# Kernel tuning notes

Measured on AMD Instinct MI355X. Metric: run time of the kernel, lower is better.

The kernel has to match this reference:

```python
import jax, jax.numpy as jnp
import numpy as np
import math

B, W, D_IN, H = 64, 512, 300, 512

def setup_inputs() -> dict:
    key = jax.random.key(0)
    ks = jax.random.split(key, 8)
    s = 1.0 / math.sqrt(D_IN)
    return {
        "char_vectors": jax.random.normal(ks[0], (B, W, D_IN), jnp.float32),
        "word_vectors": jax.random.normal(ks[1], (B, W, D_IN), jnp.float32),
        "Wk": jax.random.uniform(ks[2], (D_IN, H), jnp.float32, -s, s),
        "bk": jnp.zeros((H,), jnp.float32),
        "Wq": jax.random.uniform(ks[3], (D_IN, H), jnp.float32, -s, s),
        "bq": jnp.zeros((H,), jnp.float32),
        "Wv": jax.random.uniform(ks[4], (D_IN, H), jnp.float32, -s, s),
        "bv": jnp.zeros((H,), jnp.float32),
    }

def reference(char_vectors, word_vectors, Wk, bk, Wq, bq, Wv, bv):
    # Stack word/char reps per word -> [B, W, 2, H]
    def proj(Wm, bm):
        return jnp.stack([word_vectors @ Wm + bm, char_vectors @ Wm + bm], axis=2)
    K = proj(Wk, bk)
    Q = proj(Wq, bq)
    V = proj(Wv, bv)
    temp = jnp.sqrt(jnp.asarray(H, jnp.float32))
    # tiny 2x2 attention per word, fully batched (dropout off = eval mode)
    attn = jnp.einsum("bwqh,bwkh->bwqk", Q, K) / temp
    attn = jax.nn.softmax(attn, axis=-1)
    out = jnp.einsum("bwqk,bwkh->bwqh", attn, V)  # [B, W, 2, H]
    return out.reshape(B, W, 2 * H)
```

## Files before the change

kernel.cpp:

```cpp
#include <hip/hip_runtime.h>

#define D 300
#define HDIM 512
#define ROWS 128
#define WPB 64
#define NKS 20
#define NCH 48
#define CH_BYTES 20480
#define CH_ELEMS 10240
#define SEGW 5

typedef __attribute__((ext_vector_type(16))) float f32x16;
typedef __attribute__((ext_vector_type(4))) float f32x4;
typedef __attribute__((ext_vector_type(8))) short bf16x8;

__device__ inline unsigned short f2bf(float f) {
  unsigned int u = __float_as_uint(f);
  unsigned int r = (u + 0x7fffu + ((u >> 16) & 1u)) >> 16;
  return (unsigned short)r;
}

__device__ inline void gload_lds16(const void* g, void* l) {
  __builtin_amdgcn_global_load_lds(
      (const __attribute__((address_space(1))) unsigned int*)g,
      (__attribute__((address_space(3))) unsigned int*)l, 16, 0, 0);
}

__global__ __launch_bounds__(512) void prep_weights(
    const float* __restrict__ Wq, const float* __restrict__ Wk,
    const float* __restrict__ Wv, unsigned short* __restrict__ wt) {
  int idx = blockIdx.x * 512 + threadIdx.x;
  if (idx >= NCH * CH_ELEMS) return;
  int c = idx / CH_ELEMS, r2 = idx - c * CH_ELEMS;
  int ks = r2 >> 9, r3 = r2 & 511;
  int kh = r3 >> 8, r4 = r3 & 255;
  int col = r4 >> 3, e = r4 & 7;
  int k = ks * 16 + kh * 8 + e;
  const float* M; int gcol;
  if (c < 32) { M = (c & 1) ? Wk : Wq; gcol = (c >> 1) * 32 + col; }
  else        { M = Wv; gcol = (c - 32) * 32 + col; }
  float v = (k < D) ? M[k * HDIM + gcol] : 0.0f;
  wt[idx] = f2bf(v);
}

__global__ __launch_bounds__(256) void fused_attn(
    const float* __restrict__ charv, const float* __restrict__ wordv,
    const unsigned short* __restrict__ wt,
    const float* __restrict__ bk, const float* __restrict__ bq,
    const float* __restrict__ bv, float* __restrict__ out) {
  extern __shared__ char lds[];
  float* biasL = (float*)(lds + 3 * CH_BYTES);
  float* sS    = biasL + 1536;
  float* sAt   = sS;

  const int tid  = threadIdx.x;
  const int wid  = tid >> 6;
  const int lane = tid & 63;
  const int lo5  = lane & 31;
  const int hi   = lane >> 5;

  auto stage = [&](int t) {
    const char* src = (const char*)wt + (long)t * CH_BYTES + wid * (SEGW * 1024) + lane * 16;
    char* dst = lds + (t % 3) * CH_BYTES + wid * (SEGW * 1024);
#pragma unroll
    for (int j = 0; j < SEGW; ++j)
      gload_lds16(src + j * 1024, dst + j * 1024);
  };

  for (int i = tid; i < 1536; i += 256) {
    float v = (i < 512) ? bq[i] : ((i < 1024) ? bk[i - 512] : bv[i - 1024]);
    biasL[i] = v;
  }
  bf16x8 a[NKS];
  {
    int row = blockIdx.x * ROWS + wid * 32 + lo5;
    const float* rp = ((row & 1) ? charv : wordv) + (row >> 1) * D;
#pragma unroll
    for (int ks = 0; ks < NKS; ++ks) {
      int k0 = ks * 16 + hi * 8;
      float4 lo = {0.f, 0.f, 0.f, 0.f}, hif = {0.f, 0.f, 0.f, 0.f};
      if (k0 + 8 <= D) {
        lo  = *(const float4*)(rp + k0);
        hif = *(const float4*)(rp + k0 + 4);
      } else if (k0 < D) {
        lo  = *(const float4*)(rp + k0);
      }
      bf16x8 v;
      v[0] = (short)f2bf(lo.x);  v[1] = (short)f2bf(lo.y);
      v[2] = (short)f2bf(lo.z);  v[3] = (short)f2bf(lo.w);
      v[4] = (short)f2bf(hif.x); v[5] = (short)f2bf(hif.y);
      v[6] = (short)f2bf(hif.z); v[7] = (short)f2bf(hif.w);
      a[ks] = v;
    }
  }
  stage(0);
  stage(1);

  float p[32];
#pragma unroll
  for (int t = 0; t < 32; ++t) p[t] = 0.f;

  f32x16 accQ;

  for (int g = 0; g < 16; ++g) {
    asm volatile("s_waitcnt vmcnt(5)" ::: "memory");
    asm volatile("s_waitcnt lgkmcnt(0)" ::: "memory");
    __builtin_amdgcn_s_barrier();
    stage(2 * g + 2);
    {
      const char* base = lds + ((2 * g) % 3) * CH_BYTES + hi * 512 + lo5 * 16;
      float bqv = biasL[g * 32 + lo5];
#pragma unroll
      for (int r = 0; r < 16; ++r) accQ[r] = bqv;
#pragma unroll
      for (int ks = 0; ks < NKS; ++ks) {
        bf16x8 qb = *(const bf16x8*)(base + ks * 1024);
        accQ = __builtin_amdgcn_mfma_f32_32x32x16_bf16(a[ks], qb, accQ, 0, 0, 0);
      }
    }
    asm volatile("s_waitcnt vmcnt(5)" ::: "memory");
    asm volatile("s_waitcnt lgkmcnt(0)" ::: "memory");
    __builtin_amdgcn_s_barrier();
    stage(2 * g + 3);
    {
      const char* base = lds + ((2 * g + 1) % 3) * CH_BYTES + hi * 512 + lo5 * 16;
      float bkv = biasL[512 + g * 32 + lo5];
      f32x16 accK;
#pragma unroll
      for (int r = 0; r < 16; ++r) accK[r] = bkv;
#pragma unroll
      for (int ks = 0; ks < NKS; ++ks) {
        bf16x8 kb = *(const bf16x8*)(base + ks * 1024);
        accK = __builtin_amdgcn_mfma_f32_32x32x16_bf16(a[ks], kb, accK, 0, 0, 0);
      }
#pragma unroll
      for (int tt = 0; tt < 8; ++tt)
#pragma unroll
        for (int i = 0; i < 2; ++i)
#pragma unroll
          for (int j = 0; j < 2; ++j)
            p[tt * 4 + i * 2 + j] += accQ[2 * tt + i] * accK[2 * tt + j];
    }
  }

#pragma unroll
  for (int t = 0; t < 32; ++t) {
    float v = p[t];
    v += __shfl_xor(v, 1);
    v += __shfl_xor(v, 2);
    v += __shfl_xor(v, 4);
    v += __shfl_xor(v, 8);
    v += __shfl_xor(v, 16);
    p[t] = v;
  }
  if (lo5 == 0) {
#pragma unroll
    for (int tt = 0; tt < 8; ++tt) {
      int w = wid * 16 + (tt >> 1) * 4 + (tt & 1) + hi * 2;
#pragma unroll
      for (int q = 0; q < 4; ++q) sS[w * 4 + q] = p[tt * 4 + q];
    }
  }
  asm volatile("s_waitcnt lgkmcnt(0)" ::: "memory");
  __builtin_amdgcn_s_barrier();
  if (tid < 64) {
    const float sc = 0.044194173824159216f;
    float s[4];
#pragma unroll
    for (int t = 0; t < 4; ++t) s[t] = sS[tid * 4 + t] * sc;
#pragma unroll
    for (int i = 0; i < 2; ++i) {
      float m  = fmaxf(s[i * 2], s[i * 2 + 1]);
      float e0 = expf(s[i * 2] - m), e1 = expf(s[i * 2 + 1] - m);
      float inv = 1.0f / (e0 + e1);
      sAt[tid * 4 + i * 2]     = e0 * inv;
      sAt[tid * 4 + i * 2 + 1] = e1 * inv;
    }
  }
  asm volatile("s_waitcnt lgkmcnt(0)" ::: "memory");
  __builtin_amdgcn_s_barrier();

  f32x4 at[8];
#pragma unroll
  for (int tt = 0; tt < 8; ++tt) {
    int w = wid * 16 + (tt >> 1) * 4 + (tt & 1) + hi * 2;
    at[tt] = *(const f32x4*)(sAt + w * 4);
  }

  for (int t = 32; t < NCH; ++t) {
    if (t == 32) asm volatile("s_waitcnt vmcnt(5)" ::: "memory");
    else         asm volatile("s_waitcnt vmcnt(21)" ::: "memory");
    asm volatile("s_waitcnt lgkmcnt(0)" ::: "memory");
    __builtin_amdgcn_s_barrier();
    if (t + 2 < NCH) stage(t + 2);
    const char* base = lds + (t % 3) * CH_BYTES + hi * 512 + lo5 * 16;
    const int g = t - 32;
    float bvv = biasL[1024 + g * 32 + lo5];
    f32x16 accV;
#pragma unroll
    for (int r = 0; r < 16; ++r) accV[r] = bvv;
#pragma unroll
    for (int ks = 0; ks < NKS; ++ks) {
      bf16x8 vb = *(const bf16x8*)(base + ks * 1024);
      accV = __builtin_amdgcn_mfma_f32_32x32x16_bf16(a[ks], vb, accV, 0, 0, 0);
    }
    int h = g * 32 + lo5;
#pragma unroll
    for (int tt = 0; tt < 8; ++tt) {
      int w = wid * 16 + (tt >> 1) * 4 + (tt & 1) + hi * 2;
      long gw = (long)(blockIdx.x * WPB + w);
      float v0 = accV[2 * tt], v1 = accV[2 * tt + 1];
      out[gw * 1024 + h]       = at[tt][0] * v0 + at[tt][1] * v1;
      out[gw * 1024 + 512 + h] = at[tt][2] * v0 + at[tt][3] * v1;
    }
  }
}

extern "C" void kernel_launch(void* const* d_in, const int* in_sizes, int n_in,
                              void* d_out, int out_size, void* d_ws, size_t ws_size,
                              hipStream_t stream) {
  const float* charv = (const float*)d_in[0];
  const float* wordv = (const float*)d_in[1];
  const float* Wk = (const float*)d_in[2];
  const float* bk = (const float*)d_in[3];
  const float* Wq = (const float*)d_in[4];
  const float* bq = (const float*)d_in[5];
  const float* Wv = (const float*)d_in[6];
  const float* bv = (const float*)d_in[7];
  float* out = (float*)d_out;
  unsigned short* wt = (unsigned short*)d_ws;

  prep_weights<<<(NCH * CH_ELEMS + 511) / 512, 512, 0, stream>>>(Wq, Wk, Wv, wt);

  const int lds_bytes = 3 * CH_BYTES + 1536 * 4 + 512 * 4;
  fused_attn<<<65536 / ROWS, 256, lds_bytes, stream>>>(charv, wordv, wt, bk, bq, bv, out);
}
```

Measured before the change: 89.41 us.

## Split H across wave groups, halve rows per block, single-buffer weight chunks

```diff
diff --git a/kernel.cpp b/kernel.cpp
--- a/kernel.cpp
+++ b/kernel.cpp
@@ -2,13 +2,12 @@
 
 #define D 300
 #define HDIM 512
-#define ROWS 128
-#define WPB 64
-#define NKS 20
-#define NCH 48
-#define CH_BYTES 20480
-#define CH_ELEMS 10240
-#define SEGW 5
+#define ROWSB 64
+#define WPB 32
+#define NKS 19
+#define NCHS 24
+#define CH_BYTES 19456
+#define CH_ELEMS 9728
 
 typedef __attribute__((ext_vector_type(16))) float f32x16;
 typedef __attribute__((ext_vector_type(4))) float f32x4;
@@ -30,15 +29,16 @@
     const float* __restrict__ Wq, const float* __restrict__ Wk,
     const float* __restrict__ Wv, unsigned short* __restrict__ wt) {
   int idx = blockIdx.x * 512 + threadIdx.x;
-  if (idx >= NCH * CH_ELEMS) return;
+  if (idx >= 48 * CH_ELEMS) return;
   int c = idx / CH_ELEMS, r2 = idx - c * CH_ELEMS;
   int ks = r2 >> 9, r3 = r2 & 511;
   int kh = r3 >> 8, r4 = r3 & 255;
   int col = r4 >> 3, e = r4 & 7;
   int k = ks * 16 + kh * 8 + e;
+  int s = c / NCHS, t = c - s * NCHS;
   const float* M; int gcol;
-  if (c < 32) { M = (c & 1) ? Wk : Wq; gcol = (c >> 1) * 32 + col; }
-  else        { M = Wv; gcol = (c - 32) * 32 + col; }
+  if (t < 16) { M = (t & 1) ? Wk : Wq; gcol = (s * 8 + (t >> 1)) * 32 + col; }
+  else        { M = Wv; gcol = s * 256 + (t - 16) * 32 + col; }
   float v = (k < D) ? M[k * HDIM + gcol] : 0.0f;
   wt[idx] = f2bf(v);
 }
@@ -49,31 +49,29 @@
     const float* __restrict__ bk, const float* __restrict__ bq,
     const float* __restrict__ bv, float* __restrict__ out) {
   extern __shared__ char lds[];
-  float* biasL = (float*)(lds + 3 * CH_BYTES);
-  float* sS    = biasL + 1536;
-  float* sAt   = sS;
-
-  const int tid  = threadIdx.x;
-  const int wid  = tid >> 6;
-  const int lane = tid & 63;
-  const int lo5  = lane & 31;
-  const int hi   = lane >> 5;
+  float* sS  = (float*)(lds + 2 * CH_BYTES);
+  float* sAt = sS + 256;
+
+  const int tid   = threadIdx.x;
+  const int wid   = tid >> 6;
+  const int lane  = tid & 63;
+  const int lo5   = lane & 31;
+  const int hi    = lane >> 5;
+  const int group = wid >> 1;
+  const int rt    = wid & 1;
 
   auto stage = [&](int t) {
-    const char* src = (const char*)wt + (long)t * CH_BYTES + wid * (SEGW * 1024) + lane * 16;
-    char* dst = lds + (t % 3) * CH_BYTES + wid * (SEGW * 1024);
-#pragma unroll
-    for (int j = 0; j < SEGW; ++j)
+    const char* src = (const char*)wt + (long)(group * NCHS + t) * CH_BYTES
+                      + rt * 10240 + lane * 16;
+    char* dst = lds + group * CH_BYTES + rt * 10240;
+    const int nseg = rt ? 9 : 10;
+    for (int j = 0; j < nseg; ++j)
       gload_lds16(src + j * 1024, dst + j * 1024);
   };
 
-  for (int i = tid; i < 1536; i += 256) {
-    float v = (i < 512) ? bq[i] : ((i < 1024) ? bk[i - 512] : bv[i - 1024]);
-    biasL[i] = v;
-  }
   bf16x8 a[NKS];
   {
-    int row = blockIdx.x * ROWS + wid * 32 + lo5;
+    int row = blockIdx.x * ROWSB + rt * 32 + lo5;
     const float* rp = ((row & 1) ? charv : wordv) + (row >> 1) * D;
 #pragma unroll
     for (int ks = 0; ks < NKS; ++ks) {
@@ -94,22 +92,20 @@
     }
   }
   stage(0);
-  stage(1);
 
   float p[32];
 #pragma unroll
   for (int t = 0; t < 32; ++t) p[t] = 0.f;
 
+  const int fro = hi * 512 + lo5 * 16;
   f32x16 accQ;
 
-  for (int g = 0; g < 16; ++g) {
-    asm volatile("s_waitcnt vmcnt(5)" ::: "memory");
-    asm volatile("s_waitcnt lgkmcnt(0)" ::: "memory");
-    __builtin_amdgcn_s_barrier();
-    stage(2 * g + 2);
+  for (int g = 0; g < 8; ++g) {
+    asm volatile("s_waitcnt vmcnt(0)" ::: "memory");
+    __builtin_amdgcn_s_barrier();
     {
-      const char* base = lds + ((2 * g) % 3) * CH_BYTES + hi * 512 + lo5 * 16;
-      float bqv = biasL[g * 32 + lo5];
+      const char* base = lds + group * CH_BYTES + fro;
+      float bqv = bq[(group * 8 + g) * 32 + lo5];
 #pragma unroll
       for (int r = 0; r < 16; ++r) accQ[r] = bqv;
 #pragma unroll
@@ -118,13 +114,15 @@
         accQ = __builtin_amdgcn_mfma_f32_32x32x16_bf16(a[ks], qb, accQ, 0, 0, 0);
       }
     }
-    asm volatile("s_waitcnt vmcnt(5)" ::: "memory");
     asm volatile("s_waitcnt lgkmcnt(0)" ::: "memory");
     __builtin_amdgcn_s_barrier();
-    stage(2 * g + 3);
+    stage(2 * g + 1);
+
+    asm volatile("s_waitcnt vmcnt(0)" ::: "memory");
+    __builtin_amdgcn_s_barrier();
     {
-      const char* base = lds + ((2 * g + 1) % 3) * CH_BYTES + hi * 512 + lo5 * 16;
-      float bkv = biasL[512 + g * 32 + lo5];
+      const char* base = lds + group * CH_BYTES + fro;
+      float bkv = bk[(group * 8 + g) * 32 + lo5];
       f32x16 accK;
 #pragma unroll
       for (int r = 0; r < 16; ++r) accK[r] = bkv;
@@ -141,6 +139,9 @@
           for (int j = 0; j < 2; ++j)
             p[tt * 4 + i * 2 + j] += accQ[2 * tt + i] * accK[2 * tt + j];
     }
+    asm volatile("s_waitcnt lgkmcnt(0)" ::: "memory");
+    __builtin_amdgcn_s_barrier();
+    stage(2 * g + 2);
   }
 
 #pragma unroll
@@ -156,18 +157,18 @@
   if (lo5 == 0) {
 #pragma unroll
     for (int tt = 0; tt < 8; ++tt) {
-      int w = wid * 16 + (tt >> 1) * 4 + (tt & 1) + hi * 2;
-#pragma unroll
-      for (int q = 0; q < 4; ++q) sS[w * 4 + q] = p[tt * 4 + q];
+      int w = rt * 16 + (tt >> 1) * 4 + (tt & 1) + hi * 2;
+#pragma unroll
+      for (int q = 0; q < 4; ++q) sS[group * 128 + w * 4 + q] = p[tt * 4 + q];
     }
   }
   asm volatile("s_waitcnt lgkmcnt(0)" ::: "memory");
   __builtin_amdgcn_s_barrier();
-  if (tid < 64) {
+  if (tid < 32) {
     const float sc = 0.044194173824159216f;
     float s[4];
 #pragma unroll
-    for (int t = 0; t < 4; ++t) s[t] = sS[tid * 4 + t] * sc;
+    for (int t = 0; t < 4; ++t) s[t] = (sS[tid * 4 + t] + sS[128 + tid * 4 + t]) * sc;
 #pragma unroll
     for (int i = 0; i < 2; ++i) {
       float m  = fmaxf(s[i * 2], s[i * 2 + 1]);
@@ -183,19 +184,16 @@
   f32x4 at[8];
 #pragma unroll
   for (int tt = 0; tt < 8; ++tt) {
-    int w = wid * 16 + (tt >> 1) * 4 + (tt & 1) + hi * 2;
+    int w = rt * 16 + (tt >> 1) * 4 + (tt & 1) + hi * 2;
     at[tt] = *(const f32x4*)(sAt + w * 4);
   }
 
-  for (int t = 32; t < NCH; ++t) {
-    if (t == 32) asm volatile("s_waitcnt vmcnt(5)" ::: "memory");
-    else         asm volatile("s_waitcnt vmcnt(21)" ::: "memory");
-    asm volatile("s_waitcnt lgkmcnt(0)" ::: "memory");
-    __builtin_amdgcn_s_barrier();
-    if (t + 2 < NCH) stage(t + 2);
-    const char* base = lds + (t % 3) * CH_BYTES + hi * 512 + lo5 * 16;
-    const int g = t - 32;
-    float bvv = biasL[1024 + g * 32 + lo5];
+  for (int t = 16; t < NCHS; ++t) {
+    asm volatile("s_waitcnt vmcnt(0)" ::: "memory");
+    __builtin_amdgcn_s_barrier();
+    const char* base = lds + group * CH_BYTES + fro;
+    const int g = t - 16;
+    float bvv = bv[(group * 8 + g) * 32 + lo5];
     f32x16 accV;
 #pragma unroll
     for (int r = 0; r < 16; ++r) accV[r] = bvv;
@@ -204,14 +202,19 @@
       bf16x8 vb = *(const bf16x8*)(base + ks * 1024);
       accV = __builtin_amdgcn_mfma_f32_32x32x16_bf16(a[ks], vb, accV, 0, 0, 0);
     }
-    int h = g * 32 + lo5;
+    int h = group * 256 + g * 32 + lo5;
 #pragma unroll
     for (int tt = 0; tt < 8; ++tt) {
-      int w = wid * 16 + (tt >> 1) * 4 + (tt & 1) + hi * 2;
+      int w = rt * 16 + (tt >> 1) * 4 + (tt & 1) + hi * 2;
       long gw = (long)(blockIdx.x * WPB + w);
       float v0 = accV[2 * tt], v1 = accV[2 * tt + 1];
       out[gw * 1024 + h]       = at[tt][0] * v0 + at[tt][1] * v1;
       out[gw * 1024 + 512 + h] = at[tt][2] * v0 + at[tt][3] * v1;
+    }
+    if (t + 1 < NCHS) {
+      asm volatile("s_waitcnt lgkmcnt(0)" ::: "memory");
+      __builtin_amdgcn_s_barrier();
+      stage(t + 1);
     }
   }
 }
@@ -230,8 +233,8 @@
   float* out = (float*)d_out;
   unsigned short* wt = (unsigned short*)d_ws;
 
-  prep_weights<<<(NCH * CH_ELEMS + 511) / 512, 512, 0, stream>>>(Wq, Wk, Wv, wt);
-
-  const int lds_bytes = 3 * CH_BYTES + 1536 * 4 + 512 * 4;
-  fused_attn<<<65536 / ROWS, 256, lds_bytes, stream>>>(charv, wordv, wt, bk, bq, bv, out);
-}
+  prep_weights<<<(48 * CH_ELEMS + 511) / 512, 512, 0, stream>>>(Wq, Wk, Wv, wt);
+
+  const int lds_bytes = 2 * CH_BYTES + 256 * 4 + 128 * 4;
+  fused_attn<<<65536 / ROWSB, 256, lds_bytes, stream>>>(charv, wordv, wt, bk, bq, bv, out);
+}
```

Result: slower. 112.5 us (+25.9%).

## Swap MFMA operand roles: stage activations in LDS, stream weights from global per wave

Applied to the files above, without the earlier changes.

```diff
diff --git a/kernel.cpp b/kernel.cpp
--- a/kernel.cpp
+++ b/kernel.cpp
@@ -2,13 +2,12 @@
 
 #define D 300
 #define HDIM 512
-#define ROWS 128
+#define ROWSB 128
 #define WPB 64
-#define NKS 20
-#define NCH 48
-#define CH_BYTES 20480
-#define CH_ELEMS 10240
-#define SEGW 5
+#define NKS 19
+#define CH_BYTES 19456
+#define CH_ELEMS 9728
+#define XSTR 19456
 
 typedef __attribute__((ext_vector_type(16))) float f32x16;
 typedef __attribute__((ext_vector_type(4))) float f32x4;
@@ -20,198 +19,178 @@
   return (unsigned short)r;
 }
 
-__device__ inline void gload_lds16(const void* g, void* l) {
-  __builtin_amdgcn_global_load_lds(
-      (const __attribute__((address_space(1))) unsigned int*)g,
-      (__attribute__((address_space(3))) unsigned int*)l, 16, 0, 0);
-}
-
 __global__ __launch_bounds__(512) void prep_weights(
     const float* __restrict__ Wq, const float* __restrict__ Wk,
-    const float* __restrict__ Wv, unsigned short* __restrict__ wt) {
+    const float* __restrict__ Wv, const float* __restrict__ bq,
+    const float* __restrict__ bk, const float* __restrict__ bv,
+    unsigned short* __restrict__ wt) {
   int idx = blockIdx.x * 512 + threadIdx.x;
-  if (idx >= NCH * CH_ELEMS) return;
+  if (idx >= 48 * CH_ELEMS) return;
   int c = idx / CH_ELEMS, r2 = idx - c * CH_ELEMS;
   int ks = r2 >> 9, r3 = r2 & 511;
   int kh = r3 >> 8, r4 = r3 & 255;
   int col = r4 >> 3, e = r4 & 7;
   int k = ks * 16 + kh * 8 + e;
-  const float* M; int gcol;
-  if (c < 32) { M = (c & 1) ? Wk : Wq; gcol = (c >> 1) * 32 + col; }
-  else        { M = Wv; gcol = (c - 32) * 32 + col; }
-  float v = (k < D) ? M[k * HDIM + gcol] : 0.0f;
+  const float* M; const float* B; int gcol;
+  if (c < 16)      { M = Wq; B = bq; gcol = c * 32 + col; }
+  else if (c < 32) { M = Wk; B = bk; gcol = (c - 16) * 32 + col; }
+  else             { M = Wv; B = bv; gcol = (c - 32) * 32 + col; }
+  float v = (k < D) ? M[k * HDIM + gcol] : ((k == D) ? B[gcol] : 0.0f);
   wt[idx] = f2bf(v);
 }
 
 __global__ __launch_bounds__(256) void fused_attn(
     const float* __restrict__ charv, const float* __restrict__ wordv,
-    const unsigned short* __restrict__ wt,
-    const float* __restrict__ bk, const float* __restrict__ bq,
-    const float* __restrict__ bv, float* __restrict__ out) {
+    const unsigned short* __restrict__ wt, float* __restrict__ out) {
   extern __shared__ char lds[];
-  float* biasL = (float*)(lds + 3 * CH_BYTES);
-  float* sS    = biasL + 1536;
-  float* sAt   = sS;
+  float* sS  = (float*)(lds + 4 * XSTR);
+  float* sAt = (float*)(lds + 4 * XSTR + 2048);
 
   const int tid  = threadIdx.x;
   const int wid  = tid >> 6;
   const int lane = tid & 63;
   const int lo5  = lane & 31;
   const int hi   = lane >> 5;
-
-  auto stage = [&](int t) {
-    const char* src = (const char*)wt + (long)t * CH_BYTES + wid * (SEGW * 1024) + lane * 16;
-    char* dst = lds + (t % 3) * CH_BYTES + wid * (SEGW * 1024);
-#pragma unroll
-    for (int j = 0; j < SEGW; ++j)
-      gload_lds16(src + j * 1024, dst + j * 1024);
-  };
-
-  for (int i = tid; i < 1536; i += 256) {
-    float v = (i < 512) ? bq[i] : ((i < 1024) ? bk[i - 512] : bv[i - 1024]);
-    biasL[i] = v;
-  }
-  bf16x8 a[NKS];
-  {
-    int row = blockIdx.x * ROWS + wid * 32 + lo5;
-    const float* rp = ((row & 1) ? charv : wordv) + (row >> 1) * D;
+  const int g0   = blockIdx.x * WPB;
+
+  for (int j = tid; j < 128 * 76; j += 256) {
+    int row = j / 76, q = j - row * 76;
+    int k = q * 4;
+    ushort4 h4;
+    if (q == 75) {
+      h4.x = 0x3F80; h4.y = 0; h4.z = 0; h4.w = 0;
+    } else {
+      const float* rp = ((row & 1) ? charv : wordv) + (g0 + (row >> 1)) * D;
+      float4 v = *(const float4*)(rp + k);
+      h4.x = f2bf(v.x); h4.y = f2bf(v.y); h4.z = f2bf(v.z); h4.w = f2bf(v.w);
+    }
+    int addr = (row >> 5) * XSTR + (k >> 4) * 1024 + ((k >> 3) & 1) * 512
+               + (row & 31) * 16 + (k & 7) * 2;
+    *(ushort4*)(lds + addr) = h4;
+  }
+  __syncthreads();
+
+  const int fro = hi * 512 + lo5 * 16;
+
+  float pown[4] = {0.f, 0.f, 0.f, 0.f}, pcrs[4] = {0.f, 0.f, 0.f, 0.f};
+  for (int it = 0; it < 4; ++it) {
+    const char* qb = (const char*)wt + (long)(it * 4 + wid) * CH_BYTES + fro;
+    const char* kb = (const char*)wt + (long)(16 + it * 4 + wid) * CH_BYTES + fro;
+    bf16x8 wq[NKS], wk[NKS];
 #pragma unroll
     for (int ks = 0; ks < NKS; ++ks) {
-      int k0 = ks * 16 + hi * 8;
-      float4 lo = {0.f, 0.f, 0.f, 0.f}, hif = {0.f, 0.f, 0.f, 0.f};
-      if (k0 + 8 <= D) {
-        lo  = *(const float4*)(rp + k0);
-        hif = *(const float4*)(rp + k0 + 4);
-      } else if (k0 < D) {
-        lo  = *(const float4*)(rp + k0);
-      }
-      bf16x8 v;
-      v[0] = (short)f2bf(lo.x);  v[1] = (short)f2bf(lo.y);
-      v[2] = (short)f2bf(lo.z);  v[3] = (short)f2bf(lo.w);
-      v[4] = (short)f2bf(hif.x); v[5] = (short)f2bf(hif.y);
-      v[6] = (short)f2bf(hif.z); v[7] = (short)f2bf(hif.w);
-      a[ks] = v;
-    }
-  }
-  stage(0);
-  stage(1);
-
-  float p[32];
-#pragma unroll
-  for (int t = 0; t < 32; ++t) p[t] = 0.f;
-
-  f32x16 accQ;
-
-  for (int g = 0; g < 16; ++g) {
-    asm volatile("s_waitcnt vmcnt(5)" ::: "memory");
-    asm volatile("s_waitcnt lgkmcnt(0)" ::: "memory");
-    __builtin_amdgcn_s_barrier();
-    stage(2 * g + 2);
-    {
-      const char* base = lds + ((2 * g) % 3) * CH_BYTES + hi * 512 + lo5 * 16;
-      float bqv = biasL[g * 32 + lo5];
-#pragma unroll
-      for (int r = 0; r < 16; ++r) accQ[r] = bqv;
+      wq[ks] = *(const bf16x8*)(qb + ks * 1024);
+      wk[ks] = *(const bf16x8*)(kb + ks * 1024);
+    }
+#pragma unroll
+    for (int rg = 0; rg < 4; ++rg) {
+      const char* xb = lds + rg * XSTR + fro;
+      f32x16 accQ, accK;
+#pragma unroll
+      for (int r = 0; r < 16; ++r) { accQ[r] = 0.f; accK[r] = 0.f; }
 #pragma unroll
       for (int ks = 0; ks < NKS; ++ks) {
-        bf16x8 qb = *(const bf16x8*)(base + ks * 1024);
-        accQ = __builtin_amdgcn_mfma_f32_32x32x16_bf16(a[ks], qb, accQ, 0, 0, 0);
-      }
-    }
-    asm volatile("s_waitcnt vmcnt(5)" ::: "memory");
-    asm volatile("s_waitcnt lgkmcnt(0)" ::: "memory");
-    __builtin_amdgcn_s_barrier();
-    stage(2 * g + 3);
-    {
-      const char* base = lds + ((2 * g + 1) % 3) * CH_BYTES + hi * 512 + lo5 * 16;
-      float bkv = biasL[512 + g * 32 + lo5];
-      f32x16 accK;
-#pragma unroll
-      for (int r = 0; r < 16; ++r) accK[r] = bkv;
+        bf16x8 x = *(const bf16x8*)(xb + ks * 1024);
+        accQ = __builtin_amdgcn_mfma_f32_32x32x16_bf16(wq[ks], x, accQ, 0, 0, 0);
+        accK = __builtin_amdgcn_mfma_f32_32x32x16_bf16(wk[ks], x, accK, 0, 0, 0);
+      }
+      float down = 0.f, dcrs = 0.f;
+#pragma unroll
+      for (int r = 0; r < 16; ++r) {
+        down += accQ[r] * accK[r];
+        float ko = __shfl_xor(accK[r], 1);
+        dcrs += accQ[r] * ko;
+      }
+      pown[rg] += down;
+      pcrs[rg] += dcrs;
+    }
+  }
+#pragma unroll
+  for (int rg = 0; rg < 4; ++rg) {
+    pown[rg] += __shfl_xor(pown[rg], 32);
+    pcrs[rg] += __shfl_xor(pcrs[rg], 32);
+  }
+
+  for (int rnd = 0; rnd < 2; ++rnd) {
+    if (hi == 0) {
+#pragma unroll
+      for (int rr = 0; rr < 2; ++rr) {
+        int rg = rnd * 2 + rr;
+        int xr = rr * 32 + lo5;
+        sS[xr * 4 + wid]       = pown[rg];
+        sS[256 + xr * 4 + wid] = pcrs[rg];
+      }
+    }
+    __syncthreads();
+    if (tid < 32) {
+      float s00 = 0.f, s01 = 0.f, s10 = 0.f, s11 = 0.f;
+#pragma unroll
+      for (int wv = 0; wv < 4; ++wv) {
+        s00 += sS[(2 * tid) * 4 + wv];
+        s11 += sS[(2 * tid + 1) * 4 + wv];
+        s01 += sS[256 + (2 * tid) * 4 + wv];
+        s10 += sS[256 + (2 * tid + 1) * 4 + wv];
+      }
+      const float sc = 0.044194173824159216f;
+      s00 *= sc; s01 *= sc; s10 *= sc; s11 *= sc;
+      float m0 = fmaxf(s00, s01), m1 = fmaxf(s10, s11);
+      float e00 = expf(s00 - m0), e01 = expf(s01 - m0);
+      float e10 = expf(s10 - m1), e11 = expf(s11 - m1);
+      float i0 = 1.0f / (e00 + e01), i1 = 1.0f / (e10 + e11);
+      int w = rnd * 32 + tid;
+      sAt[w * 4 + 0] = e00 * i0;
+      sAt[w * 4 + 1] = e01 * i0;
+      sAt[w * 4 + 2] = e10 * i1;
+      sAt[w * 4 + 3] = e11 * i1;
+    }
+    __syncthreads();
+  }
+
+  for (int jt = 0; jt < 2; ++jt) {
+    const int c0 = 32 + jt * 8 + wid * 2;
+    const char* b0 = (const char*)wt + (long)c0 * CH_BYTES + fro;
+    const char* b1 = (const char*)wt + (long)(c0 + 1) * CH_BYTES + fro;
+    bf16x8 w0[NKS], w1[NKS];
+#pragma unroll
+    for (int ks = 0; ks < NKS; ++ks) {
+      w0[ks] = *(const bf16x8*)(b0 + ks * 1024);
+      w1[ks] = *(const bf16x8*)(b1 + ks * 1024);
+    }
+#pragma unroll
+    for (int rg = 0; rg < 4; ++rg) {
+      const char* xb = lds + rg * XSTR + fro;
+      f32x16 a0, a1;
+#pragma unroll
+      for (int r = 0; r < 16; ++r) { a0[r] = 0.f; a1[r] = 0.f; }
 #pragma unroll
       for (int ks = 0; ks < NKS; ++ks) {
-        bf16x8 kb = *(const bf16x8*)(base + ks * 1024);
-        accK = __builtin_amdgcn_mfma_f32_32x32x16_bf16(a[ks], kb, accK, 0, 0, 0);
-      }
-#pragma unroll
-      for (int tt = 0; tt < 8; ++tt)
-#pragma unroll
-        for (int i = 0; i < 2; ++i)
-#pragma unroll
-          for (int j = 0; j < 2; ++j)
-            p[tt * 4 + i * 2 + j] += accQ[2 * tt + i] * accK[2 * tt + j];
-    }
-  }
-
-#pragma unroll
-  for (int t = 0; t < 32; ++t) {
-    float v = p[t];
-    v += __shfl_xor(v, 1);
-    v += __shfl_xor(v, 2);
-    v += __shfl_xor(v, 4);
-    v += __shfl_xor(v, 8);
-    v += __shfl_xor(v, 16);
-    p[t] = v;
-  }
-  if (lo5 == 0) {
-#pragma unroll
-    for (int tt = 0; tt < 8; ++tt) {
-      int w = wid * 16 + (tt >> 1) * 4 + (tt & 1) + hi * 2;
-#pragma unroll
-      for (int q = 0; q < 4; ++q) sS[w * 4 + q] = p[tt * 4 + q];
-    }
-  }
-  asm volatile("s_waitcnt lgkmcnt(0)" ::: "memory");
-  __builtin_amdgcn_s_barrier();
-  if (tid < 64) {
-    const float sc = 0.044194173824159216f;
-    float s[4];
-#pragma unroll
-    for (int t = 0; t < 4; ++t) s[t] = sS[tid * 4 + t] * sc;
-#pragma unroll
-    for (int i = 0; i < 2; ++i) {
-      float m  = fmaxf(s[i * 2], s[i * 2 + 1]);
-      float e0 = expf(s[i * 2] - m), e1 = expf(s[i * 2 + 1] - m);
-      float inv = 1.0f / (e0 + e1);
-      sAt[tid * 4 + i * 2]     = e0 * inv;
-      sAt[tid * 4 + i * 2 + 1] = e1 * inv;
-    }
-  }
-  asm volatile("s_waitcnt lgkmcnt(0)" ::: "memory");
-  __builtin_amdgcn_s_barrier();
-
-  f32x4 at[8];
-#pragma unroll
-  for (int tt = 0; tt < 8; ++tt) {
-    int w = wid * 16 + (tt >> 1) * 4 + (tt & 1) + hi * 2;
-    at[tt] = *(const f32x4*)(sAt + w * 4);
-  }
-
-  for (int t = 32; t < NCH; ++t) {
-    if (t == 32) asm volatile("s_waitcnt vmcnt(5)" ::: "memory");
-    else         asm volatile("s_waitcnt vmcnt(21)" ::: "memory");
-    asm volatile("s_waitcnt lgkmcnt(0)" ::: "memory");
-    __builtin_amdgcn_s_barrier();
-    if (t + 2 < NCH) stage(t + 2);
-    const char* base = lds + (t % 3) * CH_BYTES + hi * 512 + lo5 * 16;
-    const int g = t - 32;
-    float bvv = biasL[1024 + g * 32 + lo5];
-    f32x16 accV;
-#pragma unroll
-    for (int r = 0; r < 16; ++r) accV[r] = bvv;
-#pragma unroll
-    for (int ks = 0; ks < NKS; ++ks) {
-      bf16x8 vb = *(const bf16x8*)(base + ks * 1024);
-      accV = __builtin_amdgcn_mfma_f32_32x32x16_bf16(a[ks], vb, accV, 0, 0, 0);
-    }
-    int h = g * 32 + lo5;
-#pragma unroll
-    for (int tt = 0; tt < 8; ++tt) {
-      int w = wid * 16 + (tt >> 1) * 4 + (tt & 1) + hi * 2;
-      long gw = (long)(blockIdx.x * WPB + w);
-      float v0 = accV[2 * tt], v1 = accV[2 * tt + 1];
-      out[gw * 1024 + h]       = at[tt][0] * v0 + at[tt][1] * v1;
-      out[gw * 1024 + 512 + h] = at[tt][2] * v0 + at[tt][3] * v1;
+        bf16x8 x = *(const bf16x8*)(xb + ks * 1024);
+        a0 = __builtin_amdgcn_mfma_f32_32x32x16_bf16(w0[ks], x, a0, 0, 0, 0);
+        a1 = __builtin_amdgcn_mfma_f32_32x32x16_bf16(w1[ks], x, a1, 0, 0, 0);
+      }
+      int xr = rg * 32 + lo5;
+      int w = xr >> 1;
+      f32x4 at = *(const f32x4*)(sAt + w * 4);
+      float c_own = (xr & 1) ? at[3] : at[0];
+      float c_oth = (xr & 1) ? at[2] : at[1];
+      float* obase = out + (long)(g0 + w) * 1024 + (xr & 1) * 512
+                     + jt * 256 + wid * 64 + 4 * hi;
+#pragma unroll
+      for (int set = 0; set < 2; ++set) {
+        const f32x16& av = set ? a1 : a0;
+#pragma unroll
+        for (int qd = 0; qd < 4; ++qd) {
+          float4 o;
+#pragma unroll
+          for (int e = 0; e < 4; ++e) {
+            int r = qd * 4 + e;
+            float own = av[r];
+            float oth = __shfl_xor(own, 1);
+            (&o.x)[e] = c_own * own + c_oth * oth;
+          }
+          *(float4*)(obase + set * 32 + qd * 8) = o;
+        }
+      }
     }
   }
 }
@@ -230,8 +209,8 @@
   float* out = (float*)d_out;
   unsigned short* wt = (unsigned short*)d_ws;
 
-  prep_weights<<<(NCH * CH_ELEMS + 511) / 512, 512, 0, stream>>>(Wq, Wk, Wv, wt);
-
-  const int lds_bytes = 3 * CH_BYTES + 1536 * 4 + 512 * 4;
-  fused_attn<<<65536 / ROWS, 256, lds_bytes, stream>>>(charv, wordv, wt, bk, bq, bv, out);
-}
+  prep_weights<<<48 * CH_ELEMS / 512, 512, 0, stream>>>(Wq, Wk, Wv, bq, bk, bv, wt);
+
+  const int lds_bytes = 4 * XSTR + 2048 + 1024;
+  fused_attn<<<65536 / ROWSB, 256, lds_bytes, stream>>>(charv, wordv, wt, out);
+}
```

Result: slower. 161.6 us (+80.7%).
